# Optimization experiments

Hardware: AMD Instinct MI355X
Metric: run time of the kernel (lower is better)

## Reference

```python
import jax, jax.numpy as jnp
import numpy as np

IN_NC = 7


def setup_inputs() -> dict:
    key = jax.random.key(0)
    ks = jax.random.split(key, 32)
    B, H, W = 4, 192, 192
    Cf, O, L = 64, 64, 32  # in_fea, out_fea, len=max(64//16,32)
    d = {}
    d['fea'] = jax.random.normal(ks[0], (B, Cf, H, W), jnp.float32)
    d['inputs'] = jax.random.normal(ks[1], (B, IN_NC, H, W), jnp.float32)
    j = 2
    for i in range(3):
        k = 2 * i + 1
        oc = IN_NC * 3 * k * k
        d['dw_w%d' % i] = jax.random.normal(ks[j], (Cf, 1, k, k), jnp.float32) * 0.05; j += 1
        d['dw_b%d' % i] = jnp.zeros((Cf,), jnp.float32)
        d['pw_w%d' % i] = jax.random.normal(ks[j], (oc, Cf), jnp.float32) * 0.05; j += 1
        d['pw_b%d' % i] = jnp.zeros((oc,), jnp.float32)
        d['dcn_w%d' % i] = jax.random.normal(ks[j], (O, IN_NC, k, k), jnp.float32) * 0.05; j += 1
        d['dcn_b%d' % i] = jnp.zeros((O,), jnp.float32)
    d['attn_w'] = jax.random.normal(ks[j], (O, 3 * O), jnp.float32) * 0.05; j += 1
    d['attn_b'] = jnp.zeros((O,), jnp.float32)
    d['fc_w'] = jax.random.normal(ks[j], (L, O), jnp.float32) * 0.05; j += 1
    d['fc_b'] = jnp.zeros((L,), jnp.float32)
    for i in range(3):
        d['fcs_w%d' % i] = jax.random.normal(ks[j], (O, L), jnp.float32) * 0.05; j += 1
        d['fcs_b%d' % i] = jnp.zeros((O,), jnp.float32)
    d['conv_w'] = jax.random.normal(ks[j], (O, 3 * O), jnp.float32) * 0.05; j += 1
    d['conv_b'] = jnp.zeros((O,), jnp.float32)
    return d


def _dw_conv(x, w, b):
    # depthwise conv, stride 1, SAME padding (pad = k//2 for odd k)
    y = jax.lax.conv_general_dilated(x, w, window_strides=(1, 1), padding='SAME',
                                     dimension_numbers=('NCHW', 'OIHW', 'NCHW'),
                                     feature_group_count=x.shape[1])
    return y + b[None, :, None, None]


def _pw_conv(x, w, b):
    return jnp.einsum('bchw,oc->bohw', x, w) + b[None, :, None, None]


def _mdcn(x, offset, mask, w, b, k):
    # Modulated deformable conv, deformable_groups == C (one channel per group),
    # stride 1, padding k//2. offset: [B, C*2*K, H, W] as (c, k, (dy,dx)); mask: [B, C*K, H, W].
    B, C, H, W = x.shape
    K = k * k
    pad = k // 2
    off = offset.reshape(B, C, K, 2, H, W)
    m = mask.reshape(B, C, K, H, W)
    ky = (jnp.arange(K) // k).astype(jnp.float32)
    kx = (jnp.arange(K) % k).astype(jnp.float32)
    py = off[:, :, :, 0] + (ky[:, None, None] + jnp.arange(H, dtype=jnp.float32)[None, :, None] - pad)
    px = off[:, :, :, 1] + (kx[:, None, None] + jnp.arange(W, dtype=jnp.float32)[None, None, :] - pad)
    y0 = jnp.floor(py)
    x0 = jnp.floor(px)
    wy = py - y0
    wx = px - x0
    bi = jnp.arange(B)[:, None, None, None, None]
    ci = jnp.arange(C)[None, :, None, None, None]

    def gather(yi, xi):
        valid = (yi >= 0) & (yi < H) & (xi >= 0) & (xi < W)
        yc = jnp.clip(yi, 0, H - 1).astype(jnp.int32)
        xc = jnp.clip(xi, 0, W - 1).astype(jnp.int32)
        return jnp.where(valid, x[bi, ci, yc, xc], 0.0)

    v00 = gather(y0, x0)
    v01 = gather(y0, x0 + 1)
    v10 = gather(y0 + 1, x0)
    v11 = gather(y0 + 1, x0 + 1)
    samp = (v00 * (1 - wy) * (1 - wx) + v01 * (1 - wy) * wx
            + v10 * wy * (1 - wx) + v11 * wy * wx) * m  # [B,C,K,H,W]
    O = w.shape[0]
    return jnp.einsum('bckhw,ock->bohw', samp, w.reshape(O, C, K)) + b[None, :, None, None]


def reference(fea, inputs,
              dw_w0, dw_b0, pw_w0, pw_b0, dcn_w0, dcn_b0,
              dw_w1, dw_b1, pw_w1, pw_b1, dcn_w1, dcn_b1,
              dw_w2, dw_b2, pw_w2, pw_b2, dcn_w2, dcn_b2,
              attn_w, attn_b, fc_w, fc_b,
              fcs_w0, fcs_b0, fcs_w1, fcs_b1, fcs_w2, fcs_b2,
              conv_w, conv_b):
    dw_w = [dw_w0, dw_w1, dw_w2]; dw_b = [dw_b0, dw_b1, dw_b2]
    pw_w = [pw_w0, pw_w1, pw_w2]; pw_b = [pw_b0, pw_b1, pw_b2]
    dcn_w = [dcn_w0, dcn_w1, dcn_w2]; dcn_b = [dcn_b0, dcn_b1, dcn_b2]
    fcs_w = [fcs_w0, fcs_w1, fcs_w2]; fcs_b = [fcs_b0, fcs_b1, fcs_b2]
    outs = []
    for i in range(3):
        k = 2 * i + 1
        ds = k * k
        om = _pw_conv(_dw_conv(fea, dw_w[i], dw_b[i]), pw_w[i], pw_b[i])
        offset = om[:, :IN_NC * 2 * ds]
        mask = jax.nn.sigmoid(om[:, IN_NC * 2 * ds:])
        outs.append(jax.nn.relu(_mdcn(inputs, offset, mask, dcn_w[i], dcn_b[i], k)))
    out = jnp.stack(outs, axis=1)  # [B, 3, O, H, W]
    B, T, C, H, W = out.shape
    att = jax.nn.relu(_pw_conv(out.reshape(B, T * C, H, W), attn_w, attn_b))
    att = jnp.mean(att, axis=(2, 3), keepdims=True)  # GAP -> [B, O, 1, 1]
    att = jax.nn.relu(_pw_conv(att, fc_w, fc_b))      # [B, L, 1, 1]
    atts = jnp.stack([_pw_conv(att, fcs_w[i], fcs_b[i]) for i in range(3)], axis=1)  # [B,3,O,1,1]
    out = out * atts
    out = jax.nn.relu(_pw_conv(out.reshape(B, T * C, H, W), conv_w, conv_b))
    return out
```

## Files before the change

### kernel.cpp

```cpp
#include <hip/hip_runtime.h>
#include <math.h>

#define HH 192
#define WW 192
#define HWP (192*192)
#define BB 4
#define CF 64
#define NC 7
#define OO 64
#define NTOT (BB*HWP)
#define PBLK2 (HWP/128)

typedef float f32x4 __attribute__((ext_vector_type(4)));

template<int k>
__global__ __launch_bounds__(256)
void dwv_kernel(const float* __restrict__ fea, const float* __restrict__ w,
                const float* __restrict__ bias, float* __restrict__ out) {
    constexpr int pad = k / 2;
    int idx = blockIdx.x * 256 + threadIdx.x;
    int xq = idx % 48;
    int x0 = xq * 4;
    int hpos = (idx / 48) % HH;
    int plane = idx / (48 * HH);
    int c = plane % CF;
    const float* f = fea + (size_t)plane * HWP;

    float wk[k * k];
#pragma unroll
    for (int i = 0; i < k * k; ++i) wk[i] = w[c * k * k + i];

    float acc0 = 0.f, acc1 = 0.f, acc2 = 0.f, acc3 = 0.f;
#pragma unroll
    for (int dy = 0; dy < k; ++dy) {
        int y = hpos + dy - pad;
        if (y < 0 || y >= HH) continue;
        const float* row = f + y * WW;
        float4 q0 = (x0 >= 4) ? *(const float4*)(row + x0 - 4) : make_float4(0.f, 0.f, 0.f, 0.f);
        float4 q1 = *(const float4*)(row + x0);
        float4 q2 = (x0 + 4 < WW) ? *(const float4*)(row + x0 + 4) : make_float4(0.f, 0.f, 0.f, 0.f);
        float wnd[8] = {q0.z, q0.w, q1.x, q1.y, q1.z, q1.w, q2.x, q2.y};
#pragma unroll
        for (int dx = 0; dx < k; ++dx) {
            float wt = wk[dy * k + dx];
            acc0 += wnd[0 + dx + 2 - pad] * wt;
            acc1 += wnd[1 + dx + 2 - pad] * wt;
            acc2 += wnd[2 + dx + 2 - pad] * wt;
            acc3 += wnd[3 + dx + 2 - pad] * wt;
        }
    }
    float b = bias[c];
    float4 o = make_float4(acc0 + b, acc1 + b, acc2 + b, acc3 + b);
    *(float4*)(out + (size_t)plane * HWP + hpos * WW + x0) = o;
}

__global__ void transpose_kernel(const float* __restrict__ in, float* __restrict__ out,
                                 int rows, int cols) {
    int idx = blockIdx.x * 256 + threadIdx.x;
    if (idx >= rows * cols) return;
    int r = idx / cols, c = idx % cols;
    out[c * rows + r] = in[idx];
}

__global__ void k1_fold_kernel(const float* __restrict__ pw_w, const float* __restrict__ pw_b,
                               const float* __restrict__ dw_w0, const float* __restrict__ dw_b0,
                               float* __restrict__ pw_wf, float* __restrict__ pw_bf) {
    int i = blockIdx.x * 256 + threadIdx.x;
    if (i < 21 * 64) pw_wf[i] = pw_w[i] * dw_w0[i & 63];
    if (i < 21) {
        float s = pw_b[i];
        for (int c = 0; c < 64; ++c) s += pw_w[i * 64 + c] * dw_b0[c];
        pw_bf[i] = s;
    }
}

template<int k>
__global__ __launch_bounds__(256)
void pw_sample_kernel(const float* __restrict__ pw_w, const float* __restrict__ pw_b,
                      const float* __restrict__ dw, const float* __restrict__ inputs,
                      float* __restrict__ sbuf, int tap0, int ntap, int sb_row0, int TT) {
    constexpr int K = k * k;
    constexpr int pad = k / 2;
    __shared__ float As[64][68];
    __shared__ float Bs[64][132];
    int nb0 = blockIdx.x * 128;
    int tid = threadIdx.x;
    const int M = 3 * ntap;

    {
        int m = tid & 63;
        int kq = tid >> 6;
        int srow = 0;
        if (m < M) {
            int i = m / 3, q = m - 3 * i;
            int r = tap0 + i;
            srow = (q == 2) ? (2 * TT + r) : (2 * r + q);
        }
        const float* ap = pw_w + (size_t)srow * CF;
#pragma unroll
        for (int i2 = 0; i2 < 4; ++i2) {
            int k0 = (kq * 4 + i2) * 4;
            float4 v = *(const float4*)(ap + k0);
            As[k0 + 0][m] = v.x; As[k0 + 1][m] = v.y;
            As[k0 + 2][m] = v.z; As[k0 + 3][m] = v.w;
        }
    }
    {
        int b = nb0 / HWP;
        int p0 = nb0 % HWP;
        const float* bp = dw + (size_t)b * CF * HWP + p0;
#pragma unroll
        for (int i2 = 0; i2 < 8; ++i2) {
            int idx = tid + i2 * 256;
            int kk = idx >> 5;
            int f4 = idx & 31;
            float4 v = *(const float4*)(bp + (size_t)kk * HWP + f4 * 4);
            *(float4*)&Bs[kk][f4 * 4] = v;
        }
    }
    __syncthreads();

    int tm = (tid & 15) * 4;
    int tn = (tid >> 4) * 8;
    f32x4 aA0 = 0.f, aA1 = 0.f, aB0 = 0.f, aB1 = 0.f;
    f32x4 aC0 = 0.f, aC1 = 0.f, aD0 = 0.f, aD1 = 0.f;
#pragma unroll 8
    for (int kk = 0; kk < 64; ++kk) {
        f32x4 a  = *(const f32x4*)&As[kk][tm];
        f32x4 b0 = *(const f32x4*)&Bs[kk][tn];
        f32x4 b1 = *(const f32x4*)&Bs[kk][tn + 4];
#pragma unroll
        for (int j = 0; j < 4; ++j) {
            aA0[j] += a[0] * b0[j];  aA1[j] += a[0] * b1[j];
            aB0[j] += a[1] * b0[j];  aB1[j] += a[1] * b1[j];
            aC0[j] += a[2] * b0[j];  aC1[j] += a[2] * b1[j];
            aD0[j] += a[3] * b0[j];  aD1[j] += a[3] * b1[j];
        }
    }
    __syncthreads();

    {
        f32x4 accs[8] = {aA0, aA1, aB0, aB1, aC0, aC1, aD0, aD1};
#pragma unroll
        for (int row = 0; row < 4; ++row) {
            int m = tm + row;
            if (m < M) {
                int i = m / 3, q = m - 3 * i;
                int r = tap0 + i;
                float bi = pw_b[(q == 2) ? (2 * TT + r) : (2 * r + q)];
#pragma unroll
                for (int j = 0; j < 4; ++j) {
                    Bs[m][tn + j] = accs[row * 2][j] + bi;
                    Bs[m][tn + 4 + j] = accs[row * 2 + 1][j] + bi;
                }
            }
        }
    }
    __syncthreads();

    {
        int b = nb0 / HWP;
        int p0 = nb0 % HWP;
        int j = tid & 127;
        int i0 = tid >> 7;
        int p = p0 + j;
        int h = p / WW, wq = p % WW;
        const float* inb = inputs + (size_t)b * NC * HWP;
        for (int i = i0; i < ntap; i += 2) {
            int r = tap0 + i;
            float oy = Bs[3 * i][j];
            float ox = Bs[3 * i + 1][j];
            float mr = Bs[3 * i + 2][j];
            int c = r / K;
            int kk = r - c * K;
            int ky = kk / k, kx = kk - ky * k;
            const float* inc_ = inb + (size_t)c * HWP;
            float m = 1.f / (1.f + __expf(-mr));
            float py = oy + (float)(ky + h - pad);
            float px = ox + (float)(kx + wq - pad);
            float y0 = floorf(py), x0 = floorf(px);
            float wyf = py - y0, wxf = px - x0;
            int iy0 = (int)y0, ix0 = (int)x0;
            bool y0v = (iy0 >= 0) && (iy0 < HH);
            bool y1v = (iy0 + 1 >= 0) && (iy0 + 1 < HH);
            bool x0v = (ix0 >= 0) && (ix0 < WW);
            bool x1v = (ix0 + 1 >= 0) && (ix0 + 1 < WW);
            int yc0 = min(max(iy0, 0), HH - 1), yc1 = min(max(iy0 + 1, 0), HH - 1);
            int xc0 = min(max(ix0, 0), WW - 1), xc1 = min(max(ix0 + 1, 0), WW - 1);
            float v00 = 0.f, v01 = 0.f, v10 = 0.f, v11 = 0.f;
            if (y0v) {
                if (x0v) v00 = inc_[yc0 * WW + xc0];
                if (x1v) v01 = inc_[yc0 * WW + xc1];
            }
            if (y1v) {
                if (x0v) v10 = inc_[yc1 * WW + xc0];
                if (x1v) v11 = inc_[yc1 * WW + xc1];
            }
            float s = (v00 * (1.f - wyf) * (1.f - wxf) + v01 * (1.f - wyf) * wxf +
                       v10 * wyf * (1.f - wxf) + v11 * wyf * wxf) * m;
            sbuf[(size_t)(sb_row0 + i) * NTOT + nb0 + j] = s;
        }
    }
}

__global__ __launch_bounds__(256)
void acc_gemm_kernel(const float* __restrict__ wt,
                     const float* __restrict__ bias,
                     const float* __restrict__ sbuf,
                     float* __restrict__ outbuf, int t_slot,
                     int t0, int t1, int flags) {
    __shared__ float As[64][68];
    __shared__ float Bs[64][132];
    const int T = t1 - t0;
    int nb0 = blockIdx.x * 128;
    int tid = threadIdx.x;

    for (int i4 = tid; i4 < T * 16; i4 += 256) {
        int row = i4 >> 4, c4 = (i4 & 15) * 4;
        float4 v = *(const float4*)(wt + (size_t)(t0 + row) * OO + c4);
        As[row][c4] = v.x; As[row][c4 + 1] = v.y; As[row][c4 + 2] = v.z; As[row][c4 + 3] = v.w;
    }
    for (int i4 = tid; i4 < T * 32; i4 += 256) {
        int row = i4 >> 5, f4 = (i4 & 31) * 4;
        float4 v = *(const float4*)(sbuf + (size_t)row * NTOT + nb0 + f4);
        *(float4*)&Bs[row][f4] = v;
    }
    __syncthreads();

    int tm = (tid & 15) * 4;
    int tn = (tid >> 4) * 8;
    f32x4 aA0 = 0.f, aA1 = 0.f, aB0 = 0.f, aB1 = 0.f;
    f32x4 aC0 = 0.f, aC1 = 0.f, aD0 = 0.f, aD1 = 0.f;
#pragma unroll 2
    for (int kk = 0; kk < T; ++kk) {
        f32x4 a  = *(const f32x4*)&As[kk][tm];
        f32x4 b0 = *(const f32x4*)&Bs[kk][tn];
        f32x4 b1 = *(const f32x4*)&Bs[kk][tn + 4];
#pragma unroll
        for (int j = 0; j < 4; ++j) {
            aA0[j] += a[0] * b0[j];  aA1[j] += a[0] * b1[j];
            aB0[j] += a[1] * b0[j];  aB1[j] += a[1] * b1[j];
            aC0[j] += a[2] * b0[j];  aC1[j] += a[2] * b1[j];
            aD0[j] += a[3] * b0[j];  aD1[j] += a[3] * b1[j];
        }
    }

    int b = nb0 / HWP, p0 = nb0 % HWP;
    f32x4 accs[8] = {aA0, aA1, aB0, aB1, aC0, aC1, aD0, aD1};
#pragma unroll
    for (int row = 0; row < 4; ++row) {
        int ch = tm + row;
        float* ptr = outbuf + ((size_t)((b * 3 + t_slot) * OO + ch)) * HWP + p0 + tn;
        f32x4 lo = accs[row * 2], hi = accs[row * 2 + 1];
        if (!(flags & 1)) {
            f32x4 o0 = *(const f32x4*)ptr;
            f32x4 o1 = *(const f32x4*)(ptr + 4);
#pragma unroll
            for (int j = 0; j < 4; ++j) { lo[j] += o0[j]; hi[j] += o1[j]; }
        }
        if (flags & 2) {
            float bi = bias[ch];
#pragma unroll
            for (int j = 0; j < 4; ++j) {
                lo[j] += bi; hi[j] += bi;
                lo[j] = lo[j] > 0.f ? lo[j] : 0.f;
                hi[j] = hi[j] > 0.f ? hi[j] : 0.f;
            }
        }
        *(f32x4*)ptr = lo;
        *(f32x4*)(ptr + 4) = hi;
    }
}

__global__ __launch_bounds__(256)
void attn_gemm_kernel(const float* __restrict__ outbuf, const float* __restrict__ attn_wt,
                      const float* __restrict__ attn_b, float* __restrict__ partial) {
    __shared__ float As[32][68];
    __shared__ float Bs[32][132];
    __shared__ float red[16][68];
    int nb0 = blockIdx.x * 128;
    int b = nb0 / HWP, p0 = nb0 % HWP;
    int tid = threadIdx.x;
    int tm = (tid & 15) * 4;
    int tn = (tid >> 4) * 8;

    f32x4 aA0 = 0.f, aA1 = 0.f, aB0 = 0.f, aB1 = 0.f;
    f32x4 aC0 = 0.f, aC1 = 0.f, aD0 = 0.f, aD1 = 0.f;
    for (int kc = 0; kc < 6; ++kc) {
        for (int i4 = tid; i4 < 32 * 16; i4 += 256) {
            int row = i4 >> 4, c4 = (i4 & 15) * 4;
            float4 v = *(const float4*)(attn_wt + (size_t)(kc * 32 + row) * OO + c4);
            As[row][c4] = v.x; As[row][c4 + 1] = v.y; As[row][c4 + 2] = v.z; As[row][c4 + 3] = v.w;
        }
        const float* bp = outbuf + ((size_t)(b * 192 + kc * 32)) * HWP + p0;
        for (int i4 = tid; i4 < 32 * 32; i4 += 256) {
            int row = i4 >> 5, f4 = (i4 & 31) * 4;
            float4 v = *(const float4*)(bp + (size_t)row * HWP + f4);
            *(float4*)&Bs[row][f4] = v;
        }
        __syncthreads();
#pragma unroll 4
        for (int kk = 0; kk < 32; ++kk) {
            f32x4 a  = *(const f32x4*)&As[kk][tm];
            f32x4 b0 = *(const f32x4*)&Bs[kk][tn];
            f32x4 b1 = *(const f32x4*)&Bs[kk][tn + 4];
#pragma unroll
            for (int j = 0; j < 4; ++j) {
                aA0[j] += a[0] * b0[j];  aA1[j] += a[0] * b1[j];
                aB0[j] += a[1] * b0[j];  aB1[j] += a[1] * b1[j];
                aC0[j] += a[2] * b0[j];  aC1[j] += a[2] * b1[j];
                aD0[j] += a[3] * b0[j];  aD1[j] += a[3] * b1[j];
            }
        }
        __syncthreads();
    }
    float bsum[4];
    {
        f32x4 accs[8] = {aA0, aA1, aB0, aB1, aC0, aC1, aD0, aD1};
#pragma unroll
        for (int row = 0; row < 4; ++row) {
            float bi = attn_b[tm + row];
            float s = 0.f;
#pragma unroll
            for (int j = 0; j < 4; ++j) {
                float v0 = accs[row * 2][j] + bi;
                float v1 = accs[row * 2 + 1][j] + bi;
                s += (v0 > 0.f ? v0 : 0.f) + (v1 > 0.f ? v1 : 0.f);
            }
            bsum[row] = s;
        }
    }
    int pg = tid >> 4;
#pragma unroll
    for (int row = 0; row < 4; ++row) red[pg][tm + row] = bsum[row];
    __syncthreads();
    if (tid < 64) {
        float s = 0.f;
#pragma unroll
        for (int g = 0; g < 16; ++g) s += red[g][tid];
        int lb = p0 / 128;
        partial[((size_t)(b * PBLK2 + lb)) * OO + tid] = s;
    }
}

__global__ void attn_finish_kernel(const float* __restrict__ partial,
                                   const float* __restrict__ fc_w, const float* __restrict__ fc_b,
                                   const float* __restrict__ fcs_w0, const float* __restrict__ fcs_b0,
                                   const float* __restrict__ fcs_w1, const float* __restrict__ fcs_b1,
                                   const float* __restrict__ fcs_w2, const float* __restrict__ fcs_b2,
                                   float* __restrict__ atts) {
    int b = blockIdx.x;
    __shared__ float attm[OO];
    __shared__ float fcv[32];
    int tid = threadIdx.x;
    if (tid < OO) {
        float s = 0.f;
        for (int blk = 0; blk < PBLK2; ++blk)
            s += partial[((size_t)(b * PBLK2 + blk)) * OO + tid];
        attm[tid] = s / (float)HWP;
    }
    __syncthreads();
    if (tid < 32) {
        float s = fc_b[tid];
        for (int o = 0; o < OO; ++o) s += fc_w[tid * OO + o] * attm[o];
        fcv[tid] = s > 0.f ? s : 0.f;
    }
    __syncthreads();
    if (tid < OO) {
        {
            float s = fcs_b0[tid];
            for (int j = 0; j < 32; ++j) s += fcs_w0[tid * 32 + j] * fcv[j];
            atts[b * 192 + 0 * OO + tid] = s;
        }
        {
            float s = fcs_b1[tid];
            for (int j = 0; j < 32; ++j) s += fcs_w1[tid * 32 + j] * fcv[j];
            atts[b * 192 + 1 * OO + tid] = s;
        }
        {
            float s = fcs_b2[tid];
            for (int j = 0; j < 32; ++j) s += fcs_w2[tid * 32 + j] * fcv[j];
            atts[b * 192 + 2 * OO + tid] = s;
        }
    }
}

__global__ __launch_bounds__(256)
void final_gemm_kernel(const float* __restrict__ outbuf, const float* __restrict__ atts,
                       const float* __restrict__ conv_wt, const float* __restrict__ conv_b,
                       float* __restrict__ out) {
    __shared__ float As[32][68];
    __shared__ float Bs[32][132];
    int nb0 = blockIdx.x * 128;
    int b = nb0 / HWP, p0 = nb0 % HWP;
    int tid = threadIdx.x;
    int tm = (tid & 15) * 4;
    int tn = (tid >> 4) * 8;
    const float* at = atts + b * 192;

    f32x4 aA0 = 0.f, aA1 = 0.f, aB0 = 0.f, aB1 = 0.f;
    f32x4 aC0 = 0.f, aC1 = 0.f, aD0 = 0.f, aD1 = 0.f;
    for (int kc = 0; kc < 6; ++kc) {
        for (int i4 = tid; i4 < 32 * 16; i4 += 256) {
            int row = i4 >> 4, c4 = (i4 & 15) * 4;
            float4 v = *(const float4*)(conv_wt + (size_t)(kc * 32 + row) * OO + c4);
            As[row][c4] = v.x; As[row][c4 + 1] = v.y; As[row][c4 + 2] = v.z; As[row][c4 + 3] = v.w;
        }
        const float* bp = outbuf + ((size_t)(b * 192 + kc * 32)) * HWP + p0;
        for (int i4 = tid; i4 < 32 * 32; i4 += 256) {
            int row = i4 >> 5, f4 = (i4 & 31) * 4;
            float sc = at[kc * 32 + row];
            float4 v = *(const float4*)(bp + (size_t)row * HWP + f4);
            Bs[row][f4] = v.x * sc; Bs[row][f4 + 1] = v.y * sc;
            Bs[row][f4 + 2] = v.z * sc; Bs[row][f4 + 3] = v.w * sc;
        }
        __syncthreads();
#pragma unroll 4
        for (int kk = 0; kk < 32; ++kk) {
            f32x4 a  = *(const f32x4*)&As[kk][tm];
            f32x4 b0 = *(const f32x4*)&Bs[kk][tn];
            f32x4 b1 = *(const f32x4*)&Bs[kk][tn + 4];
#pragma unroll
            for (int j = 0; j < 4; ++j) {
                aA0[j] += a[0] * b0[j];  aA1[j] += a[0] * b1[j];
                aB0[j] += a[1] * b0[j];  aB1[j] += a[1] * b1[j];
                aC0[j] += a[2] * b0[j];  aC1[j] += a[2] * b1[j];
                aD0[j] += a[3] * b0[j];  aD1[j] += a[3] * b1[j];
            }
        }
        __syncthreads();
    }
    f32x4 accs[8] = {aA0, aA1, aB0, aB1, aC0, aC1, aD0, aD1};
#pragma unroll
    for (int row = 0; row < 4; ++row) {
        int ch = tm + row;
        float bi = conv_b[ch];
        float* ptr = out + ((size_t)(b * OO + ch)) * HWP + p0 + tn;
        f32x4 lo = accs[row * 2], hi = accs[row * 2 + 1];
#pragma unroll
        for (int j = 0; j < 4; ++j) {
            lo[j] += bi; hi[j] += bi;
            lo[j] = lo[j] > 0.f ? lo[j] : 0.f;
            hi[j] = hi[j] > 0.f ? hi[j] : 0.f;
        }
        *(f32x4*)ptr = lo;
        *(f32x4*)(ptr + 4) = hi;
    }
}

extern "C" void kernel_launch(void* const* d_in, const int* in_sizes, int n_in,
                              void* d_out, int out_size, void* d_ws, size_t ws_size,
                              hipStream_t stream) {
    const float* fea    = (const float*)d_in[0];
    const float* inputs = (const float*)d_in[1];
    const float* dw_w[3]  = {(const float*)d_in[2],  (const float*)d_in[8],  (const float*)d_in[14]};
    const float* dw_b[3]  = {(const float*)d_in[3],  (const float*)d_in[9],  (const float*)d_in[15]};
    const float* pw_w[3]  = {(const float*)d_in[4],  (const float*)d_in[10], (const float*)d_in[16]};
    const float* pw_b[3]  = {(const float*)d_in[5],  (const float*)d_in[11], (const float*)d_in[17]};
    const float* dcn_w[3] = {(const float*)d_in[6],  (const float*)d_in[12], (const float*)d_in[18]};
    const float* dcn_b[3] = {(const float*)d_in[7],  (const float*)d_in[13], (const float*)d_in[19]};
    const float* attn_w = (const float*)d_in[20];
    const float* attn_b = (const float*)d_in[21];
    const float* fc_w   = (const float*)d_in[22];
    const float* fc_b   = (const float*)d_in[23];
    const float* fcs_w[3] = {(const float*)d_in[24], (const float*)d_in[26], (const float*)d_in[28]};
    const float* fcs_b[3] = {(const float*)d_in[25], (const float*)d_in[27], (const float*)d_in[29]};
    const float* conv_w = (const float*)d_in[30];
    const float* conv_b = (const float*)d_in[31];
    float* out = (float*)d_out;

    const size_t F_OUTBUF = (size_t)BB * 3 * OO * HWP;
    const size_t F_SMALL  = 73728 + 768 + 512 + 4096 + 11264 + 12288 + 12288 + 1344 + 32;
    float* W = (float*)d_ws;
    float* outbuf = W;            W += F_OUTBUF;
    size_t avail = (ws_size / 4 > F_OUTBUF + F_SMALL) ? (ws_size / 4 - F_OUTBUF - F_SMALL) : 0;
    int SB = (int)(avail / (size_t)NTOT);
    if (SB > 63) SB = 63;
    if (SB < 1) SB = 1;
    float* sbuf = W;              W += (size_t)SB * NTOT;
    float* partial = W;           W += 73728;
    float* atts = W;              W += 768;
    float* dcn_wt0 = W;           W += 512;
    float* dcn_wt1 = W;           W += 4096;
    float* dcn_wt2 = W;           W += 11264;
    float* attn_wt = W;           W += 12288;
    float* conv_wt = W;           W += 12288;
    float* pw_wf = W;             W += 1344;
    float* pw_bf = W;             W += 32;
    float* dwscr = out;

    transpose_kernel<<<(192 * 64 + 255) / 256, 256, 0, stream>>>(attn_w, attn_wt, 64, 192);
    transpose_kernel<<<(192 * 64 + 255) / 256, 256, 0, stream>>>(conv_w, conv_wt, 64, 192);
    transpose_kernel<<<(7 * 64 + 255) / 256, 256, 0, stream>>>(dcn_w[0], dcn_wt0, 64, 7);
    transpose_kernel<<<(63 * 64 + 255) / 256, 256, 0, stream>>>(dcn_w[1], dcn_wt1, 64, 63);
    transpose_kernel<<<(175 * 64 + 255) / 256, 256, 0, stream>>>(dcn_w[2], dcn_wt2, 64, 175);
    k1_fold_kernel<<<(21 * 64 + 255) / 256, 256, 0, stream>>>(pw_w[0], pw_b[0],
                                                              dw_w[0], dw_b[0], pw_wf, pw_bf);

    const int dwv_grid = (BB * CF * HH * 48) / 256;
    const int ntiles = NTOT / 128;

    dwv_kernel<5><<<dwv_grid, 256, 0, stream>>>(fea, dw_w[2], dw_b[2], dwscr);
    {
        const int TT = 175;
        for (int a0 = 0; a0 < TT; a0 += SB) {
            int a1 = (a0 + SB < TT) ? (a0 + SB) : TT;
            for (int tap0 = a0; tap0 < a1; tap0 += 21) {
                int ntap = (tap0 + 21 < a1) ? 21 : (a1 - tap0);
                pw_sample_kernel<5><<<ntiles, 256, 0, stream>>>(
                    pw_w[2], pw_b[2], dwscr, inputs, sbuf, tap0, ntap, tap0 - a0, TT);
            }
            int flags = (a0 == 0 ? 1 : 0) | (a1 == TT ? 2 : 0);
            acc_gemm_kernel<<<ntiles, 256, 0, stream>>>(dcn_wt2, dcn_b[2], sbuf, outbuf,
                                                        2, a0, a1, flags);
        }
    }
    dwv_kernel<3><<<dwv_grid, 256, 0, stream>>>(fea, dw_w[1], dw_b[1], dwscr);
    {
        const int TT = 63;
        for (int a0 = 0; a0 < TT; a0 += SB) {
            int a1 = (a0 + SB < TT) ? (a0 + SB) : TT;
            for (int tap0 = a0; tap0 < a1; tap0 += 21) {
                int ntap = (tap0 + 21 < a1) ? 21 : (a1 - tap0);
                pw_sample_kernel<3><<<ntiles, 256, 0, stream>>>(
                    pw_w[1], pw_b[1], dwscr, inputs, sbuf, tap0, ntap, tap0 - a0, TT);
            }
            int flags = (a0 == 0 ? 1 : 0) | (a1 == TT ? 2 : 0);
            acc_gemm_kernel<<<ntiles, 256, 0, stream>>>(dcn_wt1, dcn_b[1], sbuf, outbuf,
                                                        1, a0, a1, flags);
        }
    }
    {
        const int TT = 7;
        for (int a0 = 0; a0 < TT; a0 += SB) {
            int a1 = (a0 + SB < TT) ? (a0 + SB) : TT;
            for (int tap0 = a0; tap0 < a1; tap0 += 21) {
                int ntap = (tap0 + 21 < a1) ? 21 : (a1 - tap0);
                pw_sample_kernel<1><<<ntiles, 256, 0, stream>>>(
                    pw_wf, pw_bf, fea, inputs, sbuf, tap0, ntap, tap0 - a0, TT);
            }
            int flags = (a0 == 0 ? 1 : 0) | (a1 == TT ? 2 : 0);
            acc_gemm_kernel<<<ntiles, 256, 0, stream>>>(dcn_wt0, dcn_b[0], sbuf, outbuf,
                                                        0, a0, a1, flags);
        }
    }

    attn_gemm_kernel<<<NTOT / 128, 256, 0, stream>>>(outbuf, attn_wt, attn_b, partial);
    attn_finish_kernel<<<BB, 64, 0, stream>>>(partial, fc_w, fc_b,
                                              fcs_w[0], fcs_b[0], fcs_w[1], fcs_b[1],
                                              fcs_w[2], fcs_b[2], atts);
    final_gemm_kernel<<<NTOT / 128, 256, 0, stream>>>(outbuf, atts, conv_wt, conv_b, out);
}
```

Before: 753.2 us.

## Fuse pointwise offset GEMM, deformable sampling and DCN GEMM per branch

Replaces the per-chunk pw_sample and acc_gemm kernel launches with one fused kernel per branch. Each block loops over all taps in groups of 21, computing offsets and masks, sampling, and accumulating the DCN output in registers, then writes the ReLU'd result once. This removes the large sbuf scratch round-trips through global memory, the read-modify-write of outbuf, and many kernel launches. In exchange the tile width drops to 64 pixels, each block does more synchronisation steps, and it holds three 64x68 shared arrays, which may lower occupancy.

```diff
diff --git a/kernel.cpp b/kernel.cpp
--- a/kernel.cpp
+++ b/kernel.cpp
@@ -76,199 +76,163 @@
 
 template<int k>
 __global__ __launch_bounds__(256)
-void pw_sample_kernel(const float* __restrict__ pw_w, const float* __restrict__ pw_b,
-                      const float* __restrict__ dw, const float* __restrict__ inputs,
-                      float* __restrict__ sbuf, int tap0, int ntap, int sb_row0, int TT) {
+void branch_fused_kernel(const float* __restrict__ pw_w, const float* __restrict__ pw_b,
+                         const float* __restrict__ dw, const float* __restrict__ inputs,
+                         const float* __restrict__ dcn_wt, const float* __restrict__ dcn_b,
+                         float* __restrict__ outbuf, int t_slot) {
     constexpr int K = k * k;
+    constexpr int TT = NC * K;
     constexpr int pad = k / 2;
     __shared__ float As[64][68];
-    __shared__ float Bs[64][132];
-    int nb0 = blockIdx.x * 128;
+    __shared__ float Bs[64][68];
+    __shared__ float Cs[64][68];
+    int nb0 = blockIdx.x * 64;
+    int b = nb0 / HWP, p0 = nb0 % HWP;
     int tid = threadIdx.x;
-    const int M = 3 * ntap;
+    int tm = (tid & 15) * 4;
+    int tn = (tid >> 4) * 4;
+    int h0 = 0, w0 = 0;
 
     {
-        int m = tid & 63;
-        int kq = tid >> 6;
-        int srow = 0;
-        if (m < M) {
-            int i = m / 3, q = m - 3 * i;
-            int r = tap0 + i;
-            srow = (q == 2) ? (2 * TT + r) : (2 * r + q);
-        }
-        const float* ap = pw_w + (size_t)srow * CF;
-#pragma unroll
-        for (int i2 = 0; i2 < 4; ++i2) {
-            int k0 = (kq * 4 + i2) * 4;
-            float4 v = *(const float4*)(ap + k0);
-            As[k0 + 0][m] = v.x; As[k0 + 1][m] = v.y;
-            As[k0 + 2][m] = v.z; As[k0 + 3][m] = v.w;
-        }
-    }
-    {
-        int b = nb0 / HWP;
-        int p0 = nb0 % HWP;
         const float* bp = dw + (size_t)b * CF * HWP + p0;
-#pragma unroll
-        for (int i2 = 0; i2 < 8; ++i2) {
-            int idx = tid + i2 * 256;
-            int kk = idx >> 5;
-            int f4 = idx & 31;
-            float4 v = *(const float4*)(bp + (size_t)kk * HWP + f4 * 4);
-            *(float4*)&Bs[kk][f4 * 4] = v;
-        }
-    }
-    __syncthreads();
-
-    int tm = (tid & 15) * 4;
-    int tn = (tid >> 4) * 8;
-    f32x4 aA0 = 0.f, aA1 = 0.f, aB0 = 0.f, aB1 = 0.f;
-    f32x4 aC0 = 0.f, aC1 = 0.f, aD0 = 0.f, aD1 = 0.f;
-#pragma unroll 8
-    for (int kk = 0; kk < 64; ++kk) {
-        f32x4 a  = *(const f32x4*)&As[kk][tm];
-        f32x4 b0 = *(const f32x4*)&Bs[kk][tn];
-        f32x4 b1 = *(const f32x4*)&Bs[kk][tn + 4];
-#pragma unroll
-        for (int j = 0; j < 4; ++j) {
-            aA0[j] += a[0] * b0[j];  aA1[j] += a[0] * b1[j];
-            aB0[j] += a[1] * b0[j];  aB1[j] += a[1] * b1[j];
-            aC0[j] += a[2] * b0[j];  aC1[j] += a[2] * b1[j];
-            aD0[j] += a[3] * b0[j];  aD1[j] += a[3] * b1[j];
-        }
-    }
-    __syncthreads();
-
-    {
-        f32x4 accs[8] = {aA0, aA1, aB0, aB1, aC0, aC1, aD0, aD1};
-#pragma unroll
-        for (int row = 0; row < 4; ++row) {
-            int m = tm + row;
+        for (int i4 = tid; i4 < 64 * 16; i4 += 256) {
+            int kk = i4 >> 4, f4 = (i4 & 15) * 4;
+            float4 v = *(const float4*)(bp + (size_t)kk * HWP + f4);
+            *(float4*)&Bs[kk][f4] = v;
+        }
+    }
+
+    f32x4 acc0 = 0.f, acc1 = 0.f, acc2 = 0.f, acc3 = 0.f;
+    const float* inb = inputs + (size_t)b * NC * HWP;
+
+    for (int tap0 = 0; tap0 < TT; tap0 += 21) {
+        int ntap = (TT - tap0 < 21) ? (TT - tap0) : 21;
+        int M = 3 * ntap;
+        __syncthreads();
+        {
+            int m = tid & 63;
+            int kq = tid >> 6;
             if (m < M) {
                 int i = m / 3, q = m - 3 * i;
                 int r = tap0 + i;
-                float bi = pw_b[(q == 2) ? (2 * TT + r) : (2 * r + q)];
-#pragma unroll
-                for (int j = 0; j < 4; ++j) {
-                    Bs[m][tn + j] = accs[row * 2][j] + bi;
-                    Bs[m][tn + 4 + j] = accs[row * 2 + 1][j] + bi;
+                int srow = (q == 2) ? (2 * TT + r) : (2 * r + q);
+                const float* ap = pw_w + (size_t)srow * CF;
+#pragma unroll
+                for (int i2 = 0; i2 < 4; ++i2) {
+                    int k0 = (kq * 4 + i2) * 4;
+                    float4 v = *(const float4*)(ap + k0);
+                    As[k0 + 0][m] = v.x; As[k0 + 1][m] = v.y;
+                    As[k0 + 2][m] = v.z; As[k0 + 3][m] = v.w;
                 }
             }
         }
+        __syncthreads();
+        f32x4 c0 = 0.f, c1 = 0.f, c2 = 0.f, c3 = 0.f;
+#pragma unroll 8
+        for (int kk = 0; kk < 64; ++kk) {
+            f32x4 a = *(const f32x4*)&As[kk][tm];
+            f32x4 bv = *(const f32x4*)&Bs[kk][tn];
+#pragma unroll
+            for (int j = 0; j < 4; ++j) {
+                c0[j] += a[0] * bv[j]; c1[j] += a[1] * bv[j];
+                c2[j] += a[2] * bv[j]; c3[j] += a[3] * bv[j];
+            }
+        }
+        {
+            f32x4 cs[4] = {c0, c1, c2, c3};
+#pragma unroll
+            for (int r2 = 0; r2 < 4; ++r2) {
+                int m = tm + r2;
+                if (m < M) {
+                    int i = m / 3, q = m - 3 * i;
+                    int r = tap0 + i;
+                    float bi = pw_b[(q == 2) ? (2 * TT + r) : (2 * r + q)];
+                    f32x4 v = cs[r2];
+#pragma unroll
+                    for (int j = 0; j < 4; ++j) v[j] += bi;
+                    *(f32x4*)&Cs[m][tn] = v;
+                }
+            }
+        }
+        __syncthreads();
+        for (int i4 = tid; i4 < ntap * 16; i4 += 256) {
+            int row = i4 >> 4, c4 = (i4 & 15) * 4;
+            float4 v = *(const float4*)(dcn_wt + (size_t)(tap0 + row) * OO + c4);
+            *(float4*)&As[row][c4] = v;
+        }
+        {
+            int px = tid & 63;
+            int p = p0 + px;
+            int h = p / WW, wq = p % WW;
+            for (int i = tid >> 6; i < ntap; i += 4) {
+                int r = tap0 + i;
+                float oy = Cs[3 * i][px];
+                float ox = Cs[3 * i + 1][px];
+                float mr = Cs[3 * i + 2][px];
+                int c = r / K;
+                int kk2 = r - c * K;
+                int ky = kk2 / k, kx = kk2 - ky * k;
+                const float* inc_ = inb + (size_t)c * HWP;
+                float m = 1.f / (1.f + __expf(-mr));
+                float py = oy + (float)(ky + h - pad);
+                float px_ = ox + (float)(kx + wq - pad);
+                float y0 = floorf(py), x0 = floorf(px_);
+                float wyf = py - y0, wxf = px_ - x0;
+                int iy0 = (int)y0, ix0 = (int)x0;
+                bool y0v = (iy0 >= 0) && (iy0 < HH);
+                bool y1v = (iy0 + 1 >= 0) && (iy0 + 1 < HH);
+                bool x0v = (ix0 >= 0) && (ix0 < WW);
+                bool x1v = (ix0 + 1 >= 0) && (ix0 + 1 < WW);
+                int yc0 = min(max(iy0, 0), HH - 1), yc1 = min(max(iy0 + 1, 0), HH - 1);
+                int xc0 = min(max(ix0, 0), WW - 1), xc1 = min(max(ix0 + 1, 0), WW - 1);
+                float v00 = 0.f, v01 = 0.f, v10 = 0.f, v11 = 0.f;
+                if (y0v) {
+                    if (x0v) v00 = inc_[yc0 * WW + xc0];
+                    if (x1v) v01 = inc_[yc0 * WW + xc1];
+                }
+                if (y1v) {
+                    if (x0v) v10 = inc_[yc1 * WW + xc0];
+                    if (x1v) v11 = inc_[yc1 * WW + xc1];
+                }
+                float s = (v00 * (1.f - wyf) * (1.f - wxf) + v01 * (1.f - wyf) * wxf +
+                           v10 * wyf * (1.f - wxf) + v11 * wyf * wxf) * m;
+                Cs[3 * i][px] = s;
+            }
+        }
+        __syncthreads();
+        for (int kk = 0; kk < ntap; ++kk) {
+            f32x4 a = *(const f32x4*)&As[kk][tm];
+            f32x4 s = *(const f32x4*)&Cs[3 * kk][tn];
+#pragma unroll
+            for (int j = 0; j < 4; ++j) {
+                acc0[j] += a[0] * s[j]; acc1[j] += a[1] * s[j];
+                acc2[j] += a[2] * s[j]; acc3[j] += a[3] * s[j];
+            }
+        }
     }
     __syncthreads();
-
     {
-        int b = nb0 / HWP;
-        int p0 = nb0 % HWP;
-        int j = tid & 127;
-        int i0 = tid >> 7;
-        int p = p0 + j;
-        int h = p / WW, wq = p % WW;
-        const float* inb = inputs + (size_t)b * NC * HWP;
-        for (int i = i0; i < ntap; i += 2) {
-            int r = tap0 + i;
-            float oy = Bs[3 * i][j];
-            float ox = Bs[3 * i + 1][j];
-            float mr = Bs[3 * i + 2][j];
-            int c = r / K;
-            int kk = r - c * K;
-            int ky = kk / k, kx = kk - ky * k;
-            const float* inc_ = inb + (size_t)c * HWP;
-            float m = 1.f / (1.f + __expf(-mr));
-            float py = oy + (float)(ky + h - pad);
-            float px = ox + (float)(kx + wq - pad);
-            float y0 = floorf(py), x0 = floorf(px);
-            float wyf = py - y0, wxf = px - x0;
-            int iy0 = (int)y0, ix0 = (int)x0;
-            bool y0v = (iy0 >= 0) && (iy0 < HH);
-            bool y1v = (iy0 + 1 >= 0) && (iy0 + 1 < HH);
-            bool x0v = (ix0 >= 0) && (ix0 < WW);
-            bool x1v = (ix0 + 1 >= 0) && (ix0 + 1 < WW);
-            int yc0 = min(max(iy0, 0), HH - 1), yc1 = min(max(iy0 + 1, 0), HH - 1);
-            int xc0 = min(max(ix0, 0), WW - 1), xc1 = min(max(ix0 + 1, 0), WW - 1);
-            float v00 = 0.f, v01 = 0.f, v10 = 0.f, v11 = 0.f;
-            if (y0v) {
-                if (x0v) v00 = inc_[yc0 * WW + xc0];
-                if (x1v) v01 = inc_[yc0 * WW + xc1];
-            }
-            if (y1v) {
-                if (x0v) v10 = inc_[yc1 * WW + xc0];
-                if (x1v) v11 = inc_[yc1 * WW + xc1];
-            }
-            float s = (v00 * (1.f - wyf) * (1.f - wxf) + v01 * (1.f - wyf) * wxf +
-                       v10 * wyf * (1.f - wxf) + v11 * wyf * wxf) * m;
-            sbuf[(size_t)(sb_row0 + i) * NTOT + nb0 + j] = s;
-        }
-    }
-}
-
-__global__ __launch_bounds__(256)
-void acc_gemm_kernel(const float* __restrict__ wt,
-                     const float* __restrict__ bias,
-                     const float* __restrict__ sbuf,
-                     float* __restrict__ outbuf, int t_slot,
-                     int t0, int t1, int flags) {
-    __shared__ float As[64][68];
-    __shared__ float Bs[64][132];
-    const int T = t1 - t0;
-    int nb0 = blockIdx.x * 128;
-    int tid = threadIdx.x;
-
-    for (int i4 = tid; i4 < T * 16; i4 += 256) {
-        int row = i4 >> 4, c4 = (i4 & 15) * 4;
-        float4 v = *(const float4*)(wt + (size_t)(t0 + row) * OO + c4);
-        As[row][c4] = v.x; As[row][c4 + 1] = v.y; As[row][c4 + 2] = v.z; As[row][c4 + 3] = v.w;
-    }
-    for (int i4 = tid; i4 < T * 32; i4 += 256) {
-        int row = i4 >> 5, f4 = (i4 & 31) * 4;
-        float4 v = *(const float4*)(sbuf + (size_t)row * NTOT + nb0 + f4);
-        *(float4*)&Bs[row][f4] = v;
+        f32x4 accs[4] = {acc0, acc1, acc2, acc3};
+#pragma unroll
+        for (int r2 = 0; r2 < 4; ++r2) {
+            int ch = tm + r2;
+            float bi = dcn_b[ch];
+            f32x4 v = accs[r2];
+#pragma unroll
+            for (int j = 0; j < 4; ++j) {
+                v[j] += bi;
+                v[j] = v[j] > 0.f ? v[j] : 0.f;
+            }
+            *(f32x4*)&Cs[ch][tn] = v;
+        }
     }
     __syncthreads();
-
-    int tm = (tid & 15) * 4;
-    int tn = (tid >> 4) * 8;
-    f32x4 aA0 = 0.f, aA1 = 0.f, aB0 = 0.f, aB1 = 0.f;
-    f32x4 aC0 = 0.f, aC1 = 0.f, aD0 = 0.f, aD1 = 0.f;
-#pragma unroll 2
-    for (int kk = 0; kk < T; ++kk) {
-        f32x4 a  = *(const f32x4*)&As[kk][tm];
-        f32x4 b0 = *(const f32x4*)&Bs[kk][tn];
-        f32x4 b1 = *(const f32x4*)&Bs[kk][tn + 4];
-#pragma unroll
-        for (int j = 0; j < 4; ++j) {
-            aA0[j] += a[0] * b0[j];  aA1[j] += a[0] * b1[j];
-            aB0[j] += a[1] * b0[j];  aB1[j] += a[1] * b1[j];
-            aC0[j] += a[2] * b0[j];  aC1[j] += a[2] * b1[j];
-            aD0[j] += a[3] * b0[j];  aD1[j] += a[3] * b1[j];
-        }
-    }
-
-    int b = nb0 / HWP, p0 = nb0 % HWP;
-    f32x4 accs[8] = {aA0, aA1, aB0, aB1, aC0, aC1, aD0, aD1};
-#pragma unroll
-    for (int row = 0; row < 4; ++row) {
-        int ch = tm + row;
-        float* ptr = outbuf + ((size_t)((b * 3 + t_slot) * OO + ch)) * HWP + p0 + tn;
-        f32x4 lo = accs[row * 2], hi = accs[row * 2 + 1];
-        if (!(flags & 1)) {
-            f32x4 o0 = *(const f32x4*)ptr;
-            f32x4 o1 = *(const f32x4*)(ptr + 4);
-#pragma unroll
-            for (int j = 0; j < 4; ++j) { lo[j] += o0[j]; hi[j] += o1[j]; }
-        }
-        if (flags & 2) {
-            float bi = bias[ch];
-#pragma unroll
-            for (int j = 0; j < 4; ++j) {
-                lo[j] += bi; hi[j] += bi;
-                lo[j] = lo[j] > 0.f ? lo[j] : 0.f;
-                hi[j] = hi[j] > 0.f ? hi[j] : 0.f;
-            }
-        }
-        *(f32x4*)ptr = lo;
-        *(f32x4*)(ptr + 4) = hi;
+    {
+        float* op = outbuf + (size_t)((b * 3 + t_slot) * OO) * HWP + p0;
+        for (int i4 = tid; i4 < 64 * 16; i4 += 256) {
+            int row = i4 >> 4, f4 = (i4 & 15) * 4;
+            *(float4*)(op + (size_t)row * HWP + f4) = *(const float4*)&Cs[row][f4];
+        }
     }
 }
 
@@ -470,14 +434,8 @@
     float* out = (float*)d_out;
 
     const size_t F_OUTBUF = (size_t)BB * 3 * OO * HWP;
-    const size_t F_SMALL  = 73728 + 768 + 512 + 4096 + 11264 + 12288 + 12288 + 1344 + 32;
     float* W = (float*)d_ws;
     float* outbuf = W;            W += F_OUTBUF;
-    size_t avail = (ws_size / 4 > F_OUTBUF + F_SMALL) ? (ws_size / 4 - F_OUTBUF - F_SMALL) : 0;
-    int SB = (int)(avail / (size_t)NTOT);
-    if (SB > 63) SB = 63;
-    if (SB < 1) SB = 1;
-    float* sbuf = W;              W += (size_t)SB * NTOT;
     float* partial = W;           W += 73728;
     float* atts = W;              W += 768;
     float* dcn_wt0 = W;           W += 512;
@@ -498,52 +456,16 @@
                                                               dw_w[0], dw_b[0], pw_wf, pw_bf);
 
     const int dwv_grid = (BB * CF * HH * 48) / 256;
-    const int ntiles = NTOT / 128;
+    const int fuse_grid = NTOT / 64;
 
     dwv_kernel<5><<<dwv_grid, 256, 0, stream>>>(fea, dw_w[2], dw_b[2], dwscr);
-    {
-        const int TT = 175;
-        for (int a0 = 0; a0 < TT; a0 += SB) {
-            int a1 = (a0 + SB < TT) ? (a0 + SB) : TT;
-            for (int tap0 = a0; tap0 < a1; tap0 += 21) {
-                int ntap = (tap0 + 21 < a1) ? 21 : (a1 - tap0);
-                pw_sample_kernel<5><<<ntiles, 256, 0, stream>>>(
-                    pw_w[2], pw_b[2], dwscr, inputs, sbuf, tap0, ntap, tap0 - a0, TT);
-            }
-            int flags = (a0 == 0 ? 1 : 0) | (a1 == TT ? 2 : 0);
-            acc_gemm_kernel<<<ntiles, 256, 0, stream>>>(dcn_wt2, dcn_b[2], sbuf, outbuf,
-                                                        2, a0, a1, flags);
-        }
-    }
+    branch_fused_kernel<5><<<fuse_grid, 256, 0, stream>>>(
+        pw_w[2], pw_b[2], dwscr, inputs, dcn_wt2, dcn_b[2], outbuf, 2);
     dwv_kernel<3><<<dwv_grid, 256, 0, stream>>>(fea, dw_w[1], dw_b[1], dwscr);
-    {
-        const int TT = 63;
-        for (int a0 = 0; a0 < TT; a0 += SB) {
-            int a1 = (a0 + SB < TT) ? (a0 + SB) : TT;
-            for (int tap0 = a0; tap0 < a1; tap0 += 21) {
-                int ntap = (tap0 + 21 < a1) ? 21 : (a1 - tap0);
-                pw_sample_kernel<3><<<ntiles, 256, 0, stream>>>(
-                    pw_w[1], pw_b[1], dwscr, inputs, sbuf, tap0, ntap, tap0 - a0, TT);
-            }
-            int flags = (a0 == 0 ? 1 : 0) | (a1 == TT ? 2 : 0);
-            acc_gemm_kernel<<<ntiles, 256, 0, stream>>>(dcn_wt1, dcn_b[1], sbuf, outbuf,
-                                                        1, a0, a1, flags);
-        }
-    }
-    {
-        const int TT = 7;
-        for (int a0 = 0; a0 < TT; a0 += SB) {
-            int a1 = (a0 + SB < TT) ? (a0 + SB) : TT;
-            for (int tap0 = a0; tap0 < a1; tap0 += 21) {
-                int ntap = (tap0 + 21 < a1) ? 21 : (a1 - tap0);
-                pw_sample_kernel<1><<<ntiles, 256, 0, stream>>>(
-                    pw_wf, pw_bf, fea, inputs, sbuf, tap0, ntap, tap0 - a0, TT);
-            }
-            int flags = (a0 == 0 ? 1 : 0) | (a1 == TT ? 2 : 0);
-            acc_gemm_kernel<<<ntiles, 256, 0, stream>>>(dcn_wt0, dcn_b[0], sbuf, outbuf,
-                                                        0, a0, a1, flags);
-        }
-    }
+    branch_fused_kernel<3><<<fuse_grid, 256, 0, stream>>>(
+        pw_w[1], pw_b[1], dwscr, inputs, dcn_wt1, dcn_b[1], outbuf, 1);
+    branch_fused_kernel<1><<<fuse_grid, 256, 0, stream>>>(
+        pw_wf, pw_bf, fea, inputs, dcn_wt0, dcn_b[0], outbuf, 0);
 
     attn_gemm_kernel<<<NTOT / 128, 256, 0, stream>>>(outbuf, attn_wt, attn_b, partial);
     attn_finish_kernel<<<BB, 64, 0, stream>>>(partial, fc_w, fc_b,
```

After: 613.5 us. 1.23x faster.
